# Optimization experiments

Measured on AMD Instinct MI355X. Metric: run time of the kernel, lower is better.

Reference implementation:

```python
import jax, jax.numpy as jnp
import numpy as np

N_NODES = 50000
N_EDGES = 500000
IN_CH = 256
HID = 64
HEADS = 8
OUT_CH = 16
NEG_SLOPE = 0.2  # PyG GATConv default


def setup_inputs() -> dict:
    key = jax.random.key(0)
    ks = jax.random.split(key, 10)
    x = jax.random.normal(ks[0], (N_NODES, IN_CH), dtype=jnp.float32)
    edge_index = jax.random.randint(ks[1], (2, N_EDGES), 0, N_NODES, dtype=jnp.int64)
    s1 = 1.0 / np.sqrt(IN_CH)
    W1 = jax.random.uniform(ks[2], (IN_CH, HEADS * HID), jnp.float32, -s1, s1)
    att_src1 = jax.random.normal(ks[3], (HEADS, HID), dtype=jnp.float32) * 0.1
    att_dst1 = jax.random.normal(ks[4], (HEADS, HID), dtype=jnp.float32) * 0.1
    b1 = jnp.zeros((HEADS * HID,), jnp.float32)
    s2 = 1.0 / np.sqrt(HEADS * HID)
    W2 = jax.random.uniform(ks[5], (HEADS * HID, OUT_CH), jnp.float32, -s2, s2)
    att_src2 = jax.random.normal(ks[6], (1, OUT_CH), dtype=jnp.float32) * 0.1
    att_dst2 = jax.random.normal(ks[7], (1, OUT_CH), dtype=jnp.float32) * 0.1
    b2 = jnp.zeros((OUT_CH,), jnp.float32)
    return {"x": x, "edge_index": edge_index, "W1": W1, "att_src1": att_src1,
            "att_dst1": att_dst1, "b1": b1, "W2": W2, "att_src2": att_src2,
            "att_dst2": att_dst2, "b2": b2}


def _gat_conv(x, src, dst, W, att_src, att_dst, bias, heads, out_ch, concat, n_nodes):
    # Linear transform: [N, H, C]
    h = (x @ W).reshape(n_nodes, heads, out_ch)
    # Per-node attention logits: [N, H]
    a_src = jnp.einsum('nhc,hc->nh', h, att_src)
    a_dst = jnp.einsum('nhc,hc->nh', h, att_dst)
    # Edge-wise attention score (message src -> dst): [E, H]
    e = jax.nn.leaky_relu(a_src[src] + a_dst[dst], NEG_SLOPE)
    # Segment softmax over incoming edges of each destination node
    emax = jax.ops.segment_max(e, dst, num_segments=n_nodes)  # [N, H]
    emax = jnp.where(jnp.isfinite(emax), emax, 0.0)
    e = jnp.exp(e - emax[dst])
    denom = jax.ops.segment_sum(e, dst, num_segments=n_nodes)  # [N, H]
    alpha = e / (denom[dst] + 1e-16)
    # Weighted scatter-add aggregation: [N, H, C]
    msg = h[src] * alpha[:, :, None]
    out = jax.ops.segment_sum(msg, dst, num_segments=n_nodes)
    if concat:
        out = out.reshape(n_nodes, heads * out_ch)
    else:
        out = out.mean(axis=1)
    return out + bias


def reference(x, edge_index, W1, att_src1, att_dst1, b1, W2, att_src2, att_dst2, b2):
    n = x.shape[0]
    # PyG GATConv adds self-loops by default
    loops = jnp.arange(n, dtype=edge_index.dtype)
    src = jnp.concatenate([edge_index[0], loops])
    dst = jnp.concatenate([edge_index[1], loops])
    # dropout (p=0.6) is identity in eval mode
    h = _gat_conv(x, src, dst, W1, att_src1, att_dst1, b1, HEADS, HID, True, n)
    h = jax.nn.elu(h)
    out = _gat_conv(h, src, dst, W2, att_src2, att_dst2, b2, 1, OUT_CH, False, n)
    return jax.nn.log_softmax(out, axis=1)
```

## Files before the change

### kernel.cpp

```cpp
#include <hip/hip_runtime.h>
#include <math.h>

#define N_NODES 50000
#define N_EDGES 500000
#define IN_CH 256
#define D1 512
#define HEADS 8
#define HID 64
#define OUT_CH 16
#define NEG_SLOPE 0.2f

typedef __bf16 bf16x8 __attribute__((ext_vector_type(8)));
typedef float f32x4 __attribute__((ext_vector_type(4)));
typedef float f32x2 __attribute__((ext_vector_type(2)));

__device__ inline void fp8x8_to_f32(uint2 u, float* f) {
    f32x2 p0 = __builtin_amdgcn_cvt_pk_f32_fp8(u.x, false);
    f32x2 p1 = __builtin_amdgcn_cvt_pk_f32_fp8(u.x, true);
    f32x2 p2 = __builtin_amdgcn_cvt_pk_f32_fp8(u.y, false);
    f32x2 p3 = __builtin_amdgcn_cvt_pk_f32_fp8(u.y, true);
    f[0] = p0.x; f[1] = p0.y; f[2] = p1.x; f[3] = p1.y;
    f[4] = p2.x; f[5] = p2.y; f[6] = p3.x; f[7] = p3.y;
}

__device__ inline void fp8x16_to_f32(uint4 u, float* f) {
    fp8x8_to_f32(make_uint2(u.x, u.y), f);
    fp8x8_to_f32(make_uint2(u.z, u.w), f + 8);
}

__device__ inline unsigned char f32_to_fp8(float v) {
    return (unsigned char)(__builtin_amdgcn_cvt_pk_fp8_f32(v, v, 0, false) & 0xff);
}

__device__ inline float leaky_exp(float e) {
    float v = e > 0.f ? e : NEG_SLOPE * e;
    return __expf(v);
}

__device__ inline void gl_lds16(const __bf16* g, __bf16* l) {
    __builtin_amdgcn_global_load_lds(
        (const __attribute__((address_space(1))) unsigned int*)g,
        (__attribute__((address_space(3))) unsigned int*)l,
        16, 0, 0);
}

__global__ __launch_bounds__(256) void k_prep(const float* __restrict__ X,
                                              const float* __restrict__ W1,
                                              const float* __restrict__ W2,
                                              const int* __restrict__ edst,
                                              __bf16* __restrict__ Xb,
                                              __bf16* __restrict__ Wt,
                                              __bf16* __restrict__ Wt2,
                                              int* __restrict__ deg) {
    int t = blockIdx.x * 256 + threadIdx.x;
    int nthr = gridDim.x * 256;
    for (int i = t; i < N_NODES * IN_CH / 8; i += nthr) {
        size_t base = (size_t)i * 8;
        float4 v0 = *(const float4*)&X[base];
        float4 v1 = *(const float4*)&X[base + 4];
        __bf16 o[8] = {(__bf16)v0.x, (__bf16)v0.y, (__bf16)v0.z, (__bf16)v0.w,
                       (__bf16)v1.x, (__bf16)v1.y, (__bf16)v1.z, (__bf16)v1.w};
        *(uint4*)&Xb[base] = *(uint4*)o;
    }
    for (int i = t; i < D1 * IN_CH; i += nthr) {
        int n = i >> 8, k = i & 255;
        Wt[i] = (__bf16)W1[k * D1 + n];
    }
    for (int i = t; i < D1 * OUT_CH; i += nthr) {
        int n = i >> 9, k = i & 511;
        Wt2[i] = (__bf16)W2[k * OUT_CH + n];
    }
    for (int i = t; i < N_EDGES; i += nthr) atomicAdd(&deg[edst[i]], 1);
}

__global__ __launch_bounds__(256) void k_gemm1_mfma(const __bf16* __restrict__ Xb,
                                                    const __bf16* __restrict__ Wt,
                                                    const float* __restrict__ att_src,
                                                    const float* __restrict__ att_dst,
                                                    unsigned char* __restrict__ Hf8,
                                                    float* __restrict__ a_src1,
                                                    float* __restrict__ a_dst1) {
    __shared__ __align__(16) __bf16 As[128 * 64];
    __shared__ __align__(16) __bf16 Bs[128 * 64];
    int tid = threadIdx.x;
    int wid = tid >> 6, lane = tid & 63;
    int wr = wid >> 1, wc = wid & 1;
    int row0 = blockIdx.x * 128;
    int col0 = blockIdx.y * 128;
    int lq = lane >> 4;
    int lm = lane & 15;
    int sw = lm & 7;
    int r_st[4], g_st[4];
    #pragma unroll
    for (int it = 0; it < 4; ++it) {
        int idx = tid + it * 256;
        int r = idx >> 3;
        int p = idx & 7;
        r_st[it] = r;
        g_st[it] = (p ^ (r & 7)) * 8;
    }
    f32x4 acc[4][4] = {};
    for (int kt = 0; kt < IN_CH / 64; ++kt) {
        int k0 = kt * 64;
        #pragma unroll
        for (int it = 0; it < 4; ++it) {
            int idx = tid + it * 256;
            gl_lds16(&Xb[(size_t)(row0 + r_st[it]) * IN_CH + k0 + g_st[it]], &As[idx * 8]);
            gl_lds16(&Wt[(size_t)(col0 + r_st[it]) * IN_CH + k0 + g_st[it]], &Bs[idx * 8]);
        }
        __syncthreads();
        #pragma unroll
        for (int kt2 = 0; kt2 < 2; ++kt2) {
            bf16x8 af[4], bfr[4];
            #pragma unroll
            for (int i = 0; i < 4; ++i)
                af[i]  = *(bf16x8*)&As[(wr * 64 + i * 16 + lm) * 64 + (((kt2 * 4 + lq) ^ sw) * 8)];
            #pragma unroll
            for (int j = 0; j < 4; ++j)
                bfr[j] = *(bf16x8*)&Bs[(wc * 64 + j * 16 + lm) * 64 + (((kt2 * 4 + lq) ^ sw) * 8)];
            #pragma unroll
            for (int i = 0; i < 4; ++i)
                #pragma unroll
                for (int j = 0; j < 4; ++j)
                    acc[i][j] = __builtin_amdgcn_mfma_f32_16x16x32_bf16(af[i], bfr[j], acc[i][j], 0, 0, 0);
        }
        __syncthreads();
    }
    int head = blockIdx.y * 2 + wc;
    float as_v[4], ad_v[4];
    #pragma unroll
    for (int j = 0; j < 4; ++j) {
        as_v[j] = att_src[head * HID + j * 16 + lm];
        ad_v[j] = att_dst[head * HID + j * 16 + lm];
    }
    #pragma unroll
    for (int i = 0; i < 4; ++i) {
        int rbase = row0 + wr * 64 + i * 16 + lq * 4;
        #pragma unroll
        for (int r = 0; r < 4; ++r) {
            int grow = rbase + r;
            float ps = 0.f, pd = 0.f;
            #pragma unroll
            for (int j = 0; j < 4; ++j) {
                float v = acc[i][j][r];
                ps += v * as_v[j];
                pd += v * ad_v[j];
                if (grow < N_NODES)
                    Hf8[(size_t)grow * D1 + col0 + wc * 64 + j * 16 + lm] = f32_to_fp8(v);
            }
            #pragma unroll
            for (int off = 1; off < 16; off <<= 1) {
                ps += __shfl_xor(ps, off);
                pd += __shfl_xor(pd, off);
            }
            if (lm == 0 && grow < N_NODES) {
                a_src1[grow * HEADS + head] = ps;
                a_dst1[grow * HEADS + head] = pd;
            }
        }
    }
}

__global__ __launch_bounds__(1024) void k_scan1(const int* __restrict__ deg,
                                                int* __restrict__ offsets,
                                                int* __restrict__ bsum) {
    __shared__ int wsum[16];
    int tid = threadIdx.x, lane = tid & 63, wid = tid >> 6;
    int i = blockIdx.x * 1024 + tid;
    int v = (i < N_NODES) ? deg[i] : 0;
    int x = v;
    #pragma unroll
    for (int off = 1; off < 64; off <<= 1) {
        int t = __shfl_up(x, off);
        if (lane >= off) x += t;
    }
    if (lane == 63) wsum[wid] = x;
    __syncthreads();
    if (wid == 0) {
        int s = (lane < 16) ? wsum[lane] : 0;
        #pragma unroll
        for (int off = 1; off < 16; off <<= 1) {
            int t = __shfl_up(s, off);
            if (lane >= off) s += t;
        }
        if (lane < 16) wsum[lane] = s;
    }
    __syncthreads();
    int wbase = wid ? wsum[wid - 1] : 0;
    if (i < N_NODES) offsets[i] = wbase + x - v;
    if (tid == 1023) bsum[blockIdx.x] = wsum[15];
}

__global__ __launch_bounds__(256) void k_scan3(int* __restrict__ offsets,
                                               const int* __restrict__ bsum,
                                               int* __restrict__ cursor) {
    __shared__ int bpre_s[64];
    int tid = threadIdx.x;
    const int nb = (N_NODES + 1023) / 1024;
    if (tid < 64) {
        int v = (tid < nb) ? bsum[tid] : 0;
        int x = v;
        #pragma unroll
        for (int off = 1; off < 64; off <<= 1) {
            int t = __shfl_up(x, off);
            if (tid >= off) x += t;
        }
        bpre_s[tid] = x - v;
        if (blockIdx.x == 0 && tid == nb - 1) offsets[N_NODES] = x;
    }
    __syncthreads();
    int i = blockIdx.x * 256 + tid;
    if (i < N_NODES) {
        int o = offsets[i] + bpre_s[i >> 10];
        offsets[i] = o;
        cursor[i] = o;
    }
}

__global__ void k_scatter(const int* __restrict__ esrc, const int* __restrict__ edst,
                          int* __restrict__ cursor, int* __restrict__ csr) {
    int e = blockIdx.x * blockDim.x + threadIdx.x;
    if (e >= N_EDGES) return;
    int s = esrc[e], d = edst[e];
    int pos = atomicAdd(&cursor[d], 1);
    csr[pos] = s;
}

__global__ __launch_bounds__(256) void k_agg1(const unsigned char* __restrict__ Hf8,
                                              const float* __restrict__ a_src,
                                              const float* __restrict__ a_dst,
                                              const int* __restrict__ offsets,
                                              const int* __restrict__ csr,
                                              const float* __restrict__ b1,
                                              __bf16* __restrict__ OUT) {
    int wave = (blockIdx.x * blockDim.x + threadIdx.x) >> 6;
    int lane = threadIdx.x & 63;
    if (wave >= N_NODES) return;
    int d = wave;
    int half = lane >> 5;
    int l32 = lane & 31;
    int chb = l32 * 16;
    int head = l32 >> 2;
    float ad_h = a_dst[d * HEADS + head];
    float o[16];
    #pragma unroll
    for (int j = 0; j < 16; ++j) o[j] = 0.f;
    float lsum = 0.f;
    if (half == 0) {
        float wself = leaky_exp(a_src[d * HEADS + head] + ad_h);
        uint4 hu = *(const uint4*)&Hf8[(size_t)d * D1 + chb];
        float hv[16];
        fp8x16_to_f32(hu, hv);
        lsum = wself;
        #pragma unroll
        for (int j = 0; j < 16; ++j) o[j] = wself * hv[j];
    }
    int beg = offsets[d], end = offsets[d + 1];
    int idx = beg;
    for (; idx + 4 <= end; idx += 4) {
        int sA = csr[idx + half];
        int sB = csr[idx + 2 + half];
        uint4 uA = *(const uint4*)&Hf8[(size_t)sA * D1 + chb];
        uint4 uB = *(const uint4*)&Hf8[(size_t)sB * D1 + chb];
        float wA = leaky_exp(a_src[sA * HEADS + head] + ad_h);
        float wB = leaky_exp(a_src[sB * HEADS + head] + ad_h);
        float fA[16], fB[16];
        fp8x16_to_f32(uA, fA);
        fp8x16_to_f32(uB, fB);
        lsum += wA + wB;
        #pragma unroll
        for (int j = 0; j < 16; ++j) o[j] += wA * fA[j] + wB * fB[j];
    }
    for (; idx < end; idx += 2) {
        int e = idx + half;
        bool valid = e < end;
        int s = valid ? csr[e] : csr[idx];
        uint4 u = *(const uint4*)&Hf8[(size_t)s * D1 + chb];
        float w = valid ? leaky_exp(a_src[s * HEADS + head] + ad_h) : 0.f;
        float f[16];
        fp8x16_to_f32(u, f);
        lsum += w;
        #pragma unroll
        for (int j = 0; j < 16; ++j) o[j] += w * f[j];
    }
    #pragma unroll
    for (int j = 0; j < 16; ++j) o[j] += __shfl_xor(o[j], 32);
    lsum += __shfl_xor(lsum, 32);
    if (half == 0) {
        float inv = 1.0f / (lsum + 1e-16f);
        __bf16 r[16];
        #pragma unroll
        for (int j = 0; j < 16; ++j) {
            float v = o[j] * inv + b1[chb + j];
            v = v > 0.f ? v : (__expf(v) - 1.0f);
            r[j] = (__bf16)v;
        }
        *(uint4*)&OUT[(size_t)d * D1 + chb]     = *(uint4*)&r[0];
        *(uint4*)&OUT[(size_t)d * D1 + chb + 8] = *(uint4*)&r[8];
    }
}

__global__ __launch_bounds__(256) void k_gemm2_mfma(const __bf16* __restrict__ A,
                                                    const __bf16* __restrict__ Wt2,
                                                    const float* __restrict__ as2v,
                                                    const float* __restrict__ ad2v,
                                                    __bf16* __restrict__ H2,
                                                    float* __restrict__ a_src2,
                                                    float* __restrict__ a_dst2) {
    int tid = threadIdx.x;
    int wid = tid >> 6, lane = tid & 63;
    int lq = lane >> 4, lm = lane & 15;
    int row0 = blockIdx.x * 64 + wid * 16;
    int arow = row0 + lm;
    const __bf16* ap = A + (size_t)(arow < N_NODES ? arow : 0) * D1;
    f32x4 acc = {};
    #pragma unroll
    for (int k0 = 0; k0 < 16; ++k0) {
        bf16x8 af  = *(const bf16x8*)&ap[k0 * 32 + lq * 8];
        bf16x8 bfr = *(const bf16x8*)&Wt2[lm * D1 + k0 * 32 + lq * 8];
        acc = __builtin_amdgcn_mfma_f32_16x16x32_bf16(af, bfr, acc, 0, 0, 0);
    }
    float as_c = as2v[lm], ad_c = ad2v[lm];
    #pragma unroll
    for (int r = 0; r < 4; ++r) {
        int gr = row0 + lq * 4 + r;
        float v = acc[r];
        if (gr < N_NODES) H2[gr * OUT_CH + lm] = (__bf16)v;
        float ps = v * as_c, pd = v * ad_c;
        #pragma unroll
        for (int off = 1; off < 16; off <<= 1) {
            ps += __shfl_xor(ps, off);
            pd += __shfl_xor(pd, off);
        }
        if (lm == 0 && gr < N_NODES) { a_src2[gr] = ps; a_dst2[gr] = pd; }
    }
}

__global__ __launch_bounds__(256) void k_agg2(const __bf16* __restrict__ H2,
                                              const float* __restrict__ a_src,
                                              const float* __restrict__ a_dst,
                                              const int* __restrict__ offsets,
                                              const int* __restrict__ csr,
                                              const float* __restrict__ b2,
                                              float* __restrict__ OUT) {
    int wave = (blockIdx.x * blockDim.x + threadIdx.x) >> 6;
    int lane = threadIdx.x & 63;
    if (wave >= N_NODES) return;
    int d = wave;
    int g = lane >> 4, c = lane & 15;
    float ad = a_dst[d];
    float o = 0.f, lsum = 0.f;
    if (g == 0) {
        float wself = leaky_exp(a_src[d] + ad);
        o = wself * (float)H2[d * OUT_CH + c];
        lsum = wself;
    }
    int beg = offsets[d], end = offsets[d + 1];
    int i0 = beg + g;
    for (; i0 + 4 < end; i0 += 8) {
        int s0 = csr[i0], s1 = csr[i0 + 4];
        float h0 = (float)H2[s0 * OUT_CH + c];
        float h1 = (float)H2[s1 * OUT_CH + c];
        float wt0 = leaky_exp(a_src[s0] + ad);
        float wt1 = leaky_exp(a_src[s1] + ad);
        lsum += wt0 + wt1;
        o += wt0 * h0 + wt1 * h1;
    }
    for (; i0 < end; i0 += 4) {
        int s = csr[i0];
        float wt = leaky_exp(a_src[s] + ad);
        float h = (float)H2[s * OUT_CH + c];
        lsum += wt;
        o += wt * h;
    }
    o += __shfl_xor(o, 16);  o += __shfl_xor(o, 32);
    lsum += __shfl_xor(lsum, 16);  lsum += __shfl_xor(lsum, 32);
    float v = o / (lsum + 1e-16f) + b2[c];
    float mx = v;
    #pragma unroll
    for (int off = 1; off < 16; off <<= 1) mx = fmaxf(mx, __shfl_xor(mx, off));
    float se = __expf(v - mx);
    #pragma unroll
    for (int off = 1; off < 16; off <<= 1) se += __shfl_xor(se, off);
    float res = v - mx - logf(se);
    if (lane < 16) OUT[d * OUT_CH + lane] = res;
}

extern "C" void kernel_launch(void* const* d_in, const int* in_sizes, int n_in,
                              void* d_out, int out_size, void* d_ws, size_t ws_size,
                              hipStream_t stream) {
    const float* x        = (const float*)d_in[0];
    const int*   ei       = (const int*)d_in[1];
    const float* W1       = (const float*)d_in[2];
    const float* att_src1 = (const float*)d_in[3];
    const float* att_dst1 = (const float*)d_in[4];
    const float* b1       = (const float*)d_in[5];
    const float* W2       = (const float*)d_in[6];
    const float* att_src2 = (const float*)d_in[7];
    const float* att_dst2 = (const float*)d_in[8];
    const float* b2       = (const float*)d_in[9];
    float* out = (float*)d_out;

    const int* esrc = ei;
    const int* edst = ei + N_EDGES;

    char* ws = (char*)d_ws;
    size_t off = 0;
    auto alloc = [&](size_t bytes) { char* p = ws + off; off = (off + bytes + 255) & ~(size_t)255; return p; };
    unsigned char* Hf8 = (unsigned char*)alloc((size_t)N_NODES * D1);
    __bf16* out1   = (__bf16*)alloc((size_t)N_NODES * D1 * 2);
    __bf16* Xb     = (__bf16*)alloc((size_t)N_NODES * IN_CH * 2);
    __bf16* Wt     = (__bf16*)alloc((size_t)D1 * IN_CH * 2);
    __bf16* Wt2    = (__bf16*)alloc((size_t)D1 * OUT_CH * 2);
    float* a_src1  = (float*)alloc((size_t)N_NODES * HEADS * 4);
    float* a_dst1  = (float*)alloc((size_t)N_NODES * HEADS * 4);
    __bf16* h2     = (__bf16*)alloc((size_t)N_NODES * OUT_CH * 2);
    float* a_src2  = (float*)alloc((size_t)N_NODES * 4);
    float* a_dst2  = (float*)alloc((size_t)N_NODES * 4);
    int*   deg     = (int*)alloc((size_t)N_NODES * 4);
    int*   offsets = (int*)alloc((size_t)(N_NODES + 1) * 4);
    int*   cursor  = (int*)alloc((size_t)N_NODES * 4);
    int*   csr     = (int*)alloc((size_t)N_EDGES * 4);
    int*   bsum    = (int*)alloc(64 * 4);
    (void)ws_size;

    hipMemsetAsync(deg, 0, (size_t)N_NODES * 4, stream);
    k_prep<<<512, 256, 0, stream>>>(x, W1, W2, edst, Xb, Wt, Wt2, deg);
    dim3 g1((N_NODES + 127) / 128, D1 / 128);
    k_gemm1_mfma<<<g1, 256, 0, stream>>>(Xb, Wt, att_src1, att_dst1, Hf8, a_src1, a_dst1);
    int nb = (N_NODES + 1023) / 1024;
    k_scan1<<<nb, 1024, 0, stream>>>(deg, offsets, bsum);
    k_scan3<<<(N_NODES + 255) / 256, 256, 0, stream>>>(offsets, bsum, cursor);
    k_scatter<<<(N_EDGES + 255) / 256, 256, 0, stream>>>(esrc, edst, cursor, csr);
    k_agg1<<<(N_NODES * 64 + 255) / 256, 256, 0, stream>>>(Hf8, a_src1, a_dst1, offsets, csr, b1, out1);
    k_gemm2_mfma<<<(N_NODES + 63) / 64, 256, 0, stream>>>(out1, Wt2, att_src2, att_dst2, h2, a_src2, a_dst2);
    k_agg2<<<(N_NODES * 64 + 255) / 256, 256, 0, stream>>>(h2, a_src2, a_dst2, offsets, csr, b2, out);
}
```

Baseline: 286.5 us.

## Fuse edge scatter into GEMM1 launch and prefetch CSR indices in aggregations

The first-layer GEMM and the CSR scatter now run in one launch. The grid is flattened to 1D and the extra blocks perform the atomic scatter, so the memory-bound scatter can overlap with the compute-bound GEMM and one launch is removed. The scan kernels are moved ahead of the GEMM so the cursor is ready for the fused launch. Both aggregation kernels also software-pipeline their loops by loading the next CSR source indices before processing the current pair. In exchange, the GEMM and scatter blocks now contend for the GPU, and the extra registers held by the prefetch could lower occupancy.

```diff
diff --git a/kernel.cpp b/kernel.cpp
--- a/kernel.cpp
+++ b/kernel.cpp
@@ -9,6 +9,10 @@
 #define HID 64
 #define OUT_CH 16
 #define NEG_SLOPE 0.2f
+
+#define G1_BX 391
+#define G1_BLOCKS (G1_BX * 4)
+#define SCAT_BLOCKS ((N_EDGES + 255) / 256)
 
 typedef __bf16 bf16x8 __attribute__((ext_vector_type(8)));
 typedef float f32x4 __attribute__((ext_vector_type(4)));
@@ -73,20 +77,33 @@
     for (int i = t; i < N_EDGES; i += nthr) atomicAdd(&deg[edst[i]], 1);
 }
 
-__global__ __launch_bounds__(256) void k_gemm1_mfma(const __bf16* __restrict__ Xb,
-                                                    const __bf16* __restrict__ Wt,
-                                                    const float* __restrict__ att_src,
-                                                    const float* __restrict__ att_dst,
-                                                    unsigned char* __restrict__ Hf8,
-                                                    float* __restrict__ a_src1,
-                                                    float* __restrict__ a_dst1) {
+__global__ __launch_bounds__(256) void k_gemm1s(const __bf16* __restrict__ Xb,
+                                                const __bf16* __restrict__ Wt,
+                                                const float* __restrict__ att_src,
+                                                const float* __restrict__ att_dst,
+                                                unsigned char* __restrict__ Hf8,
+                                                float* __restrict__ a_src1,
+                                                float* __restrict__ a_dst1,
+                                                const int* __restrict__ esrc,
+                                                const int* __restrict__ edst,
+                                                int* __restrict__ cursor,
+                                                int* __restrict__ csr) {
     __shared__ __align__(16) __bf16 As[128 * 64];
     __shared__ __align__(16) __bf16 Bs[128 * 64];
+    if (blockIdx.x >= G1_BLOCKS) {
+        int e = (blockIdx.x - G1_BLOCKS) * 256 + threadIdx.x;
+        if (e < N_EDGES) {
+            int s = esrc[e], d = edst[e];
+            int pos = atomicAdd(&cursor[d], 1);
+            csr[pos] = s;
+        }
+        return;
+    }
     int tid = threadIdx.x;
     int wid = tid >> 6, lane = tid & 63;
     int wr = wid >> 1, wc = wid & 1;
-    int row0 = blockIdx.x * 128;
-    int col0 = blockIdx.y * 128;
+    int row0 = (blockIdx.x % G1_BX) * 128;
+    int col0 = (blockIdx.x / G1_BX) * 128;
     int lq = lane >> 4;
     int lm = lane & 15;
     int sw = lm & 7;
@@ -126,7 +143,7 @@
         }
         __syncthreads();
     }
-    int head = blockIdx.y * 2 + wc;
+    int head = (blockIdx.x / G1_BX) * 2 + wc;
     float as_v[4], ad_v[4];
     #pragma unroll
     for (int j = 0; j < 4; ++j) {
@@ -217,13 +234,20 @@
     }
 }
 
-__global__ void k_scatter(const int* __restrict__ esrc, const int* __restrict__ edst,
-                          int* __restrict__ cursor, int* __restrict__ csr) {
-    int e = blockIdx.x * blockDim.x + threadIdx.x;
-    if (e >= N_EDGES) return;
-    int s = esrc[e], d = edst[e];
-    int pos = atomicAdd(&cursor[d], 1);
-    csr[pos] = s;
+__device__ inline void agg1_pair(const unsigned char* __restrict__ Hf8,
+                                 const float* __restrict__ a_src,
+                                 int sA, int sB, int chb, int head, float ad_h,
+                                 float* o, float& lsum) {
+    uint4 uA = *(const uint4*)&Hf8[(size_t)sA * D1 + chb];
+    uint4 uB = *(const uint4*)&Hf8[(size_t)sB * D1 + chb];
+    float wA = leaky_exp(a_src[sA * HEADS + head] + ad_h);
+    float wB = leaky_exp(a_src[sB * HEADS + head] + ad_h);
+    float fA[16], fB[16];
+    fp8x16_to_f32(uA, fA);
+    fp8x16_to_f32(uB, fB);
+    lsum += wA + wB;
+    #pragma unroll
+    for (int j = 0; j < 16; ++j) o[j] += wA * fA[j] + wB * fB[j];
 }
 
 __global__ __launch_bounds__(256) void k_agg1(const unsigned char* __restrict__ Hf8,
@@ -257,19 +281,17 @@
     }
     int beg = offsets[d], end = offsets[d + 1];
     int idx = beg;
-    for (; idx + 4 <= end; idx += 4) {
+    if (idx + 4 <= end) {
         int sA = csr[idx + half];
         int sB = csr[idx + 2 + half];
-        uint4 uA = *(const uint4*)&Hf8[(size_t)sA * D1 + chb];
-        uint4 uB = *(const uint4*)&Hf8[(size_t)sB * D1 + chb];
-        float wA = leaky_exp(a_src[sA * HEADS + head] + ad_h);
-        float wB = leaky_exp(a_src[sB * HEADS + head] + ad_h);
-        float fA[16], fB[16];
-        fp8x16_to_f32(uA, fA);
-        fp8x16_to_f32(uB, fB);
-        lsum += wA + wB;
-        #pragma unroll
-        for (int j = 0; j < 16; ++j) o[j] += wA * fA[j] + wB * fB[j];
+        for (; idx + 8 <= end; idx += 4) {
+            int sA2 = csr[idx + 4 + half];
+            int sB2 = csr[idx + 6 + half];
+            agg1_pair(Hf8, a_src, sA, sB, chb, head, ad_h, o, lsum);
+            sA = sA2; sB = sB2;
+        }
+        agg1_pair(Hf8, a_src, sA, sB, chb, head, ad_h, o, lsum);
+        idx += 4;
     }
     for (; idx < end; idx += 2) {
         int e = idx + half;
@@ -334,6 +356,18 @@
         }
         if (lm == 0 && gr < N_NODES) { a_src2[gr] = ps; a_dst2[gr] = pd; }
     }
+}
+
+__device__ inline void agg2_pair(const __bf16* __restrict__ H2,
+                                 const float* __restrict__ a_src,
+                                 int s0, int s1, int c, float ad,
+                                 float& o, float& lsum) {
+    float h0 = (float)H2[s0 * OUT_CH + c];
+    float h1 = (float)H2[s1 * OUT_CH + c];
+    float wt0 = leaky_exp(a_src[s0] + ad);
+    float wt1 = leaky_exp(a_src[s1] + ad);
+    lsum += wt0 + wt1;
+    o += wt0 * h0 + wt1 * h1;
 }
 
 __global__ __launch_bounds__(256) void k_agg2(const __bf16* __restrict__ H2,
@@ -357,14 +391,15 @@
     }
     int beg = offsets[d], end = offsets[d + 1];
     int i0 = beg + g;
-    for (; i0 + 4 < end; i0 += 8) {
+    if (i0 + 4 < end) {
         int s0 = csr[i0], s1 = csr[i0 + 4];
-        float h0 = (float)H2[s0 * OUT_CH + c];
-        float h1 = (float)H2[s1 * OUT_CH + c];
-        float wt0 = leaky_exp(a_src[s0] + ad);
-        float wt1 = leaky_exp(a_src[s1] + ad);
-        lsum += wt0 + wt1;
-        o += wt0 * h0 + wt1 * h1;
+        for (; i0 + 12 < end; i0 += 8) {
+            int t0 = csr[i0 + 8], t1 = csr[i0 + 12];
+            agg2_pair(H2, a_src, s0, s1, c, ad, o, lsum);
+            s0 = t0; s1 = t1;
+        }
+        agg2_pair(H2, a_src, s0, s1, c, ad, o, lsum);
+        i0 += 8;
     }
     for (; i0 < end; i0 += 4) {
         int s = csr[i0];
@@ -426,12 +461,11 @@
 
     hipMemsetAsync(deg, 0, (size_t)N_NODES * 4, stream);
     k_prep<<<512, 256, 0, stream>>>(x, W1, W2, edst, Xb, Wt, Wt2, deg);
-    dim3 g1((N_NODES + 127) / 128, D1 / 128);
-    k_gemm1_mfma<<<g1, 256, 0, stream>>>(Xb, Wt, att_src1, att_dst1, Hf8, a_src1, a_dst1);
     int nb = (N_NODES + 1023) / 1024;
     k_scan1<<<nb, 1024, 0, stream>>>(deg, offsets, bsum);
     k_scan3<<<(N_NODES + 255) / 256, 256, 0, stream>>>(offsets, bsum, cursor);
-    k_scatter<<<(N_EDGES + 255) / 256, 256, 0, stream>>>(esrc, edst, cursor, csr);
+    k_gemm1s<<<G1_BLOCKS + SCAT_BLOCKS, 256, 0, stream>>>(
+        Xb, Wt, att_src1, att_dst1, Hf8, a_src1, a_dst1, esrc, edst, cursor, csr);
     k_agg1<<<(N_NODES * 64 + 255) / 256, 256, 0, stream>>>(Hf8, a_src1, a_dst1, offsets, csr, b1, out1);
     k_gemm2_mfma<<<(N_NODES + 63) / 64, 256, 0, stream>>>(out1, Wt2, att_src2, att_dst2, h2, a_src2, a_dst2);
     k_agg2<<<(N_NODES * 64 + 255) / 256, 256, 0, stream>>>(h2, a_src2, a_dst2, offsets, csr, b2, out);
```

New measurement: 288.3 us. Within noise of the previous version (+0.6%).
